# Kernel optimization log

Measured on AMD Instinct MI355X. Metric: run time of the kernel, lower is better.

The kernel has to match this reference:

```python
import jax, jax.numpy as jnp
import numpy as np

B, S, D, H, E, K = 4, 1024, 1024, 4096, 8, 2

def setup_inputs() -> dict:
    key = jax.random.key(0)
    ks = jax.random.split(key, 6)
    sd = 1.0 / np.sqrt(D)
    sh = 1.0 / np.sqrt(H)
    return {
        "x": jax.random.normal(ks[0], (B, S, D), jnp.float32),
        "Wg": jax.random.normal(ks[1], (D, E), jnp.float32) * sd,
        "bg": jnp.zeros((E,), jnp.float32),
        "W1": jax.random.normal(ks[2], (E, D, H), jnp.float32) * sd,
        "b1": jnp.zeros((E, H), jnp.float32),
        "Wa": jax.random.normal(ks[3], (E, D, H), jnp.float32) * sd,
        "ba": jnp.zeros((E, H), jnp.float32),
        "W2": jax.random.normal(ks[4], (E, H, D), jnp.float32) * sh,
        "b2": jnp.zeros((E, D), jnp.float32),
        "kv_cache": 0,
    }

def reference(x, Wg, bg, W1, b1, Wa, ba, W2, b2, kv_cache):
    # gate: softmax over experts, top-k, renormalize
    gate = jax.nn.softmax(x @ Wg + bg, axis=-1)            # [B,S,E]
    w, idx = jax.lax.top_k(gate, K)                        # [B,S,K]
    w = w / jnp.sum(w, axis=-1, keepdims=True)
    # dense all-expert FF with SwiGLU: fc2( silu(fc_a(x)) * fc1(x) )
    a = jnp.einsum('bsd,edh->bseh', x, Wa) + ba            # [B,S,E,H]
    g = a * jax.nn.sigmoid(a)
    u = jnp.einsum('bsd,edh->bseh', x, W1) + b1
    y = jnp.einsum('bseh,ehd->bsed', g * u, W2) + b2       # [B,S,E,D]
    # gather top-k experts per token and combine
    sel = jnp.take_along_axis(y, idx[..., None], axis=2)   # [B,S,K,D]
    out = jnp.sum(sel * w[..., None], axis=-2)             # [B,S,D]
    return out
```

## Files before the change

### kernel.cpp

```cpp
#include <hip/hip_runtime.h>
#include <hip/hip_bf16.h>
#include <math.h>

#define TOKENS 4096
#define DD 1024
#define HH 4096
#define NE 8
#define PAIRS 8192
#define ROWCAP 8448
#define TILE_CAP 40
#define G1_NT 16
#define G2_NT 32

typedef __bf16 bf16x8 __attribute__((ext_vector_type(8)));
typedef float f32x4 __attribute__((ext_vector_type(4)));

__device__ __forceinline__ unsigned short f2bf(float f) {
  union { float f; unsigned int u; } c; c.f = f;
  unsigned int x = c.u;
  return (unsigned short)((x + 0x7fffu + ((x >> 16) & 1u)) >> 16);
}

__device__ __forceinline__ void lds16(void* l, const void* g) {
  __builtin_amdgcn_global_load_lds((const __attribute__((address_space(1))) void*)g,
                                   (__attribute__((address_space(3))) void*)l, 16, 0, 0);
}

__global__ void init_kernel(int* counts) {
  if (threadIdx.x < NE) counts[threadIdx.x] = 0;
}

__global__ __launch_bounds__(256) void transpose_kernel(const float* __restrict__ in,
                                                        unsigned short* __restrict__ out,
                                                        int R, int C) {
  int ntr = R >> 6, ntc = C >> 6;
  int per_e = ntr * ntc;
  int b = blockIdx.x;
  int e = b / per_e;
  int rem = b - e * per_e;
  int tr = rem / ntc, tc = rem - (rem / ntc) * ntc;
  const float* ie = in + (size_t)e * R * C;
  unsigned short* oe = out + (size_t)e * R * C;

  __shared__ float t[64][68];
  int tid = threadIdx.x;
  int lr = tid >> 2;
  int c4 = (tid & 3) << 4;
  const float* src = ie + (size_t)(tr * 64 + lr) * C + tc * 64 + c4;
  float4 v0 = *(const float4*)(src);
  float4 v1 = *(const float4*)(src + 4);
  float4 v2 = *(const float4*)(src + 8);
  float4 v3 = *(const float4*)(src + 12);
  *(float4*)&t[lr][c4] = v0;
  *(float4*)&t[lr][c4 + 4] = v1;
  *(float4*)&t[lr][c4 + 8] = v2;
  *(float4*)&t[lr][c4 + 12] = v3;
  __syncthreads();

  int oc = tid >> 2;
  int r0 = (tid & 3) << 4;
  unsigned int pk[8];
#pragma unroll
  for (int i = 0; i < 8; i++) {
    unsigned int lo = f2bf(t[r0 + 2 * i][oc]);
    unsigned int hi = f2bf(t[r0 + 2 * i + 1][oc]);
    pk[i] = lo | (hi << 16);
  }
  unsigned short* dst = oe + (size_t)(tc * 64 + oc) * R + tr * 64 + r0;
  *(uint4*)(dst) = make_uint4(pk[0], pk[1], pk[2], pk[3]);
  *(uint4*)(dst + 8) = make_uint4(pk[4], pk[5], pk[6], pk[7]);
}

__global__ __launch_bounds__(256) void gate_kernel(const float* __restrict__ x,
    const float* __restrict__ Wg, const float* __restrict__ bg,
    int* __restrict__ counts, int* __restrict__ tok_e, int* __restrict__ tok_slot,
    float* __restrict__ tok_w) {
  int t = blockIdx.x, tid = threadIdx.x;
  const float* xr = x + (size_t)t * DD;
  float p[8] = {0, 0, 0, 0, 0, 0, 0, 0};
  for (int d = tid; d < DD; d += 256) {
    float xv = xr[d];
    const float4* wrow = (const float4*)(Wg + (size_t)d * NE);
    float4 w0 = wrow[0], w1 = wrow[1];
    p[0] += xv * w0.x; p[1] += xv * w0.y; p[2] += xv * w0.z; p[3] += xv * w0.w;
    p[4] += xv * w1.x; p[5] += xv * w1.y; p[6] += xv * w1.z; p[7] += xv * w1.w;
  }
#pragma unroll
  for (int e = 0; e < 8; e++) {
    p[e] += __shfl_down(p[e], 32);
    p[e] += __shfl_down(p[e], 16);
    p[e] += __shfl_down(p[e], 8);
    p[e] += __shfl_down(p[e], 4);
    p[e] += __shfl_down(p[e], 2);
    p[e] += __shfl_down(p[e], 1);
  }
  __shared__ float red[4][8];
  if ((tid & 63) == 0) {
#pragma unroll
    for (int e = 0; e < 8; e++) red[tid >> 6][e] = p[e];
  }
  __syncthreads();
  if (tid == 0) {
    float l[8];
#pragma unroll
    for (int e = 0; e < 8; e++) l[e] = red[0][e] + red[1][e] + red[2][e] + red[3][e] + bg[e];
    int e0 = 0; float l0 = l[0];
    for (int e = 1; e < 8; e++) if (l[e] > l0) { e0 = e; l0 = l[e]; }
    int e1 = -1; float l1 = -3.4e38f;
    for (int e = 0; e < 8; e++) if (e != e0 && l[e] > l1) { e1 = e; l1 = l[e]; }
    float w0 = 1.f / (1.f + __expf(l1 - l0));
    float w1 = 1.f - w0;
    int s0 = atomicAdd(&counts[e0], 1);
    int s1 = atomicAdd(&counts[e1], 1);
    tok_e[2 * t] = e0;     tok_slot[2 * t] = s0;     tok_w[2 * t] = w0;
    tok_e[2 * t + 1] = e1; tok_slot[2 * t + 1] = s1; tok_w[2 * t + 1] = w1;
  }
}

__global__ void scan_kernel(const int* __restrict__ counts, int* __restrict__ offsets,
                            int* __restrict__ tm_e, int* __restrict__ tm_row0,
                            int* __restrict__ tm_nrow, int* __restrict__ ntp) {
  if (threadIdx.x != 0 || blockIdx.x != 0) return;
  int c[NE];
#pragma unroll
  for (int e = 0; e < NE; e++) c[e] = counts[e];
  int off = 0, nt = 0;
  for (int e = 0; e < NE; e++) {
    offsets[e] = off;
    for (int r = 0; r < c[e]; r += 256) {
      tm_e[nt] = e;
      tm_row0[nt] = off + r;
      tm_nrow[nt] = (c[e] - r < 256) ? (c[e] - r) : 256;
      nt++;
    }
    off += c[e];
  }
  *ntp = nt;
}

__global__ __launch_bounds__(64) void gather_kernel(const float* __restrict__ x,
    const int* __restrict__ tok_e, const int* __restrict__ tok_slot,
    const float* __restrict__ tok_w, const int* __restrict__ offsets,
    unsigned short* __restrict__ Xe, int* __restrict__ pair_row, float* __restrict__ rw) {
  int pp = blockIdx.x, tid = threadIdx.x;
  int e = tok_e[pp];
  int row = offsets[e] + tok_slot[pp];
  int t = pp >> 1;
  const float* src = x + (size_t)t * DD + tid * 16;
  float4 v0 = *(const float4*)(src);
  float4 v1 = *(const float4*)(src + 4);
  float4 v2 = *(const float4*)(src + 8);
  float4 v3 = *(const float4*)(src + 12);
  unsigned int pk[8];
  pk[0] = f2bf(v0.x) | ((unsigned int)f2bf(v0.y) << 16);
  pk[1] = f2bf(v0.z) | ((unsigned int)f2bf(v0.w) << 16);
  pk[2] = f2bf(v1.x) | ((unsigned int)f2bf(v1.y) << 16);
  pk[3] = f2bf(v1.z) | ((unsigned int)f2bf(v1.w) << 16);
  pk[4] = f2bf(v2.x) | ((unsigned int)f2bf(v2.y) << 16);
  pk[5] = f2bf(v2.z) | ((unsigned int)f2bf(v2.w) << 16);
  pk[6] = f2bf(v3.x) | ((unsigned int)f2bf(v3.y) << 16);
  pk[7] = f2bf(v3.z) | ((unsigned int)f2bf(v3.w) << 16);
  unsigned short* dst = Xe + (size_t)row * DD + tid * 16;
  *(uint4*)(dst) = make_uint4(pk[0], pk[1], pk[2], pk[3]);
  *(uint4*)(dst + 8) = make_uint4(pk[4], pk[5], pk[6], pk[7]);
  if (tid == 0) { pair_row[pp] = row; rw[row] = tok_w[pp]; }
}

__global__ __launch_bounds__(512, 2) void gemm1_kernel(
    const unsigned short* __restrict__ Xe,
    const unsigned short* __restrict__ WaT,
    const unsigned short* __restrict__ W1T,
    const float* __restrict__ ba, const float* __restrict__ b1,
    unsigned short* __restrict__ h,
    const int* __restrict__ tm_e, const int* __restrict__ tm_row0,
    const int* __restrict__ tm_nrow, const int* __restrict__ ntp) {
  __shared__ unsigned short sm[8][8192];

  int work = blockIdx.x;
  int tile = work >> 5;
  if (tile >= *ntp) return;
  int n0 = (work & 31) << 7;
  int e = tm_e[tile], row0 = tm_row0[tile], nrow = tm_nrow[tile];

  int tid = threadIdx.x;
  int lane = tid & 63, wid = tid >> 6;
  int wm = wid >> 2, wn = wid & 3;
  int fr = lane & 15, kc = lane >> 4;

  const unsigned short* gA  = Xe + (size_t)row0 * DD;
  const unsigned short* gA1 = gA + (size_t)128 * DD;
  const unsigned short* gBa = WaT + ((size_t)e << 22) + (size_t)n0 * DD;
  const unsigned short* gBu = W1T + ((size_t)e << 22) + (size_t)n0 * DD;

  int srow = tid >> 3;
  int sx0 = (((tid & 7) ^ (srow & 7)) << 3);

  auto stg = [&](int tt, int slot, const unsigned short* gsrc) {
    int c = tt < G1_NT ? tt : G1_NT - 1;
    unsigned short* L = &sm[((tt & 1) << 2) | slot][0];
    const unsigned short* s = gsrc + (size_t)srow * DD + (c << 6) + sx0;
    lds16(L + (size_t)tid * 8, s);
    lds16(L + (size_t)(tid + 512) * 8, s + (size_t)64 * DD);
  };
  auto fragp = [&](int buf, int slot, int r, int ks) {
    return (const bf16x8*)(&sm[(buf << 2) | slot][0] + r * 64 +
                           ((((ks << 2) | kc) ^ (r & 7)) << 3));
  };

  f32x4 accA[8][2], accU[8][2];
  f32x4 z = {0.f, 0.f, 0.f, 0.f};
#pragma unroll
  for (int m = 0; m < 8; m++)
#pragma unroll
    for (int n = 0; n < 2; n++) { accA[m][n] = z; accU[m][n] = z; }

  stg(0, 2, gBa); stg(0, 3, gBu); stg(0, 0, gA); stg(0, 1, gA1);
  stg(1, 2, gBa); stg(1, 3, gBu); stg(1, 0, gA);
  asm volatile("s_waitcnt vmcnt(6)\ns_barrier" ::: "memory");

  for (int T = 0; T < G1_NT; ++T) {
    int buf = T & 1;
    bf16x8 a[4][2], bA[2][2], bU[2][2];
#pragma unroll
    for (int m = 0; m < 4; m++)
#pragma unroll
      for (int ks = 0; ks < 2; ks++) {
        int R = wm * 128 + m * 16 + fr;
        a[m][ks] = *fragp(buf, R >> 7, R & 127, ks);
      }
#pragma unroll
    for (int n = 0; n < 2; n++)
#pragma unroll
      for (int ks = 0; ks < 2; ks++)
        bA[n][ks] = *fragp(buf, 2, wn * 32 + n * 16 + fr, ks);
    stg(T + 1, 1, gA1);
    __builtin_amdgcn_s_setprio(1);
#pragma unroll
    for (int m = 0; m < 4; m++)
#pragma unroll
      for (int n = 0; n < 2; n++)
#pragma unroll
        for (int ks = 0; ks < 2; ks++)
          accA[m][n] = __builtin_amdgcn_mfma_f32_16x16x32_bf16(a[m][ks], bA[n][ks], accA[m][n], 0, 0, 0);
    __builtin_amdgcn_s_setprio(0);
    asm volatile("s_waitcnt lgkmcnt(0)\ns_barrier" ::: "memory");
#pragma unroll
    for (int n = 0; n < 2; n++)
#pragma unroll
      for (int ks = 0; ks < 2; ks++)
        bU[n][ks] = *fragp(buf, 3, wn * 32 + n * 16 + fr, ks);
    stg(T + 2, 2, gBa);
    __builtin_amdgcn_s_setprio(1);
#pragma unroll
    for (int m = 0; m < 4; m++)
#pragma unroll
      for (int n = 0; n < 2; n++)
#pragma unroll
        for (int ks = 0; ks < 2; ks++)
          accU[m][n] = __builtin_amdgcn_mfma_f32_16x16x32_bf16(a[m][ks], bU[n][ks], accU[m][n], 0, 0, 0);
    __builtin_amdgcn_s_setprio(0);
    asm volatile("s_waitcnt lgkmcnt(0)\ns_barrier" ::: "memory");
#pragma unroll
    for (int m = 0; m < 4; m++)
#pragma unroll
      for (int ks = 0; ks < 2; ks++) {
        int R = wm * 128 + 64 + m * 16 + fr;
        a[m][ks] = *fragp(buf, R >> 7, R & 127, ks);
      }
    stg(T + 2, 3, gBu);
    __builtin_amdgcn_s_setprio(1);
#pragma unroll
    for (int m = 0; m < 4; m++)
#pragma unroll
      for (int n = 0; n < 2; n++)
#pragma unroll
        for (int ks = 0; ks < 2; ks++)
          accA[4 + m][n] = __builtin_amdgcn_mfma_f32_16x16x32_bf16(a[m][ks], bA[n][ks], accA[4 + m][n], 0, 0, 0);
    __builtin_amdgcn_s_setprio(0);
    asm volatile("s_waitcnt lgkmcnt(0)\ns_barrier" ::: "memory");
    stg(T + 2, 0, gA);
    __builtin_amdgcn_s_setprio(1);
#pragma unroll
    for (int m = 0; m < 4; m++)
#pragma unroll
      for (int n = 0; n < 2; n++)
#pragma unroll
        for (int ks = 0; ks < 2; ks++)
          accU[4 + m][n] = __builtin_amdgcn_mfma_f32_16x16x32_bf16(a[m][ks], bU[n][ks], accU[4 + m][n], 0, 0, 0);
    __builtin_amdgcn_s_setprio(0);
    asm volatile("s_waitcnt vmcnt(6)\ns_barrier" ::: "memory");
  }

  int lr4 = kc * 4;
#pragma unroll
  for (int n = 0; n < 2; n++) {
    int col = n0 + wn * 32 + n * 16 + fr;
    float bav = ba[e * HH + col];
    float buv = b1[e * HH + col];
#pragma unroll
    for (int m = 0; m < 8; m++) {
#pragma unroll
      for (int j = 0; j < 4; j++) {
        int r = wm * 128 + m * 16 + lr4 + j;
        if (r < nrow) {
          float av = accA[m][n][j] + bav;
          float uv = accU[m][n][j] + buv;
          float s = __builtin_amdgcn_rcpf(1.f + __expf(-av));
          h[(size_t)(row0 + r) * HH + col] = f2bf(av * s * uv);
        }
      }
    }
  }
}

__global__ __launch_bounds__(512, 2) void gemm2_kernel(
    const unsigned short* __restrict__ hb,
    const unsigned short* __restrict__ W2T,
    const float* __restrict__ b2, const float* __restrict__ rw,
    float* __restrict__ contribA, float* __restrict__ contribB,
    const int* __restrict__ tm_e, const int* __restrict__ tm_row0,
    const int* __restrict__ tm_nrow, const int* __restrict__ ntp) {
  __shared__ unsigned short sm[9][8192];

  int work = blockIdx.x;
  int tile = work >> 4;
  if (tile >= *ntp) return;
  int rem = work & 15;
  int n0 = (rem >> 1) << 7;
  int kh = rem & 1;
  int e = tm_e[tile], row0 = tm_row0[tile], nrow = tm_nrow[tile];

  int tid = threadIdx.x;
  int lane = tid & 63, wid = tid >> 6;
  int wm = wid >> 2, wn = wid & 3;
  int fr = lane & 15, kc = lane >> 4;

  const unsigned short* gA = hb + (size_t)row0 * HH + kh * 2048;
  const unsigned short* gB = W2T + ((size_t)e << 22) + (size_t)n0 * HH + kh * 2048;

  int srow = tid >> 3;
  int sx0 = (((tid & 7) ^ (srow & 7)) << 3);

  auto stgA = [&](int tt) {
    int c = tt < G2_NT ? tt : G2_NT - 1;
    int sl = (tt % 3) << 1;
    const unsigned short* s = gA + (size_t)srow * HH + (c << 6) + sx0;
    lds16(&sm[sl][0] + (size_t)tid * 8, s);
    lds16(&sm[sl][0] + (size_t)(tid + 512) * 8, s + (size_t)64 * HH);
    lds16(&sm[sl + 1][0] + (size_t)tid * 8, s + (size_t)128 * HH);
    lds16(&sm[sl + 1][0] + (size_t)(tid + 512) * 8, s + (size_t)192 * HH);
  };
  auto stgB = [&](int tt) {
    int c = tt < G2_NT ? tt : G2_NT - 1;
    unsigned short* L = &sm[6 + tt % 3][0];
    const unsigned short* s = gB + (size_t)srow * HH + (c << 6) + sx0;
    lds16(L + (size_t)tid * 8, s);
    lds16(L + (size_t)(tid + 512) * 8, s + (size_t)64 * HH);
  };
  auto fragp = [&](int slot, int r, int ks) {
    return (const bf16x8*)(&sm[slot][0] + r * 64 + ((((ks << 2) | kc) ^ (r & 7)) << 3));
  };

  f32x4 acc[8][2];
  f32x4 z = {0.f, 0.f, 0.f, 0.f};
#pragma unroll
  for (int m = 0; m < 8; m++)
#pragma unroll
    for (int n = 0; n < 2; n++) acc[m][n] = z;

  stgB(0); stgA(0); stgB(1); stgA(1); stgB(2);
  asm volatile("s_waitcnt vmcnt(6)\ns_barrier" ::: "memory");

  for (int T = 0; T < G2_NT; ++T) {
    int slA = (T % 3) << 1;
    int slB = 6 + T % 3;
    bf16x8 a[4][2], b[2][2];
#pragma unroll
    for (int m = 0; m < 4; m++)
#pragma unroll
      for (int ks = 0; ks < 2; ks++) {
        int R = wm * 128 + m * 16 + fr;
        a[m][ks] = *fragp(slA + (R >> 7), R & 127, ks);
      }
#pragma unroll
    for (int n = 0; n < 2; n++)
#pragma unroll
      for (int ks = 0; ks < 2; ks++)
        b[n][ks] = *fragp(slB, wn * 32 + n * 16 + fr, ks);
    stgA(T + 2);
    __builtin_amdgcn_s_setprio(1);
#pragma unroll
    for (int m = 0; m < 4; m++)
#pragma unroll
      for (int n = 0; n < 2; n++)
#pragma unroll
        for (int ks = 0; ks < 2; ks++)
          acc[m][n] = __builtin_amdgcn_mfma_f32_16x16x32_bf16(a[m][ks], b[n][ks], acc[m][n], 0, 0, 0);
    __builtin_amdgcn_s_setprio(0);
    asm volatile("s_waitcnt lgkmcnt(0)\ns_barrier" ::: "memory");
#pragma unroll
    for (int m = 0; m < 4; m++)
#pragma unroll
      for (int ks = 0; ks < 2; ks++) {
        int R = wm * 128 + 64 + m * 16 + fr;
        a[m][ks] = *fragp(slA + (R >> 7), R & 127, ks);
      }
    stgB(T + 3);
    __builtin_amdgcn_s_setprio(1);
#pragma unroll
    for (int m = 0; m < 4; m++)
#pragma unroll
      for (int n = 0; n < 2; n++)
#pragma unroll
        for (int ks = 0; ks < 2; ks++)
          acc[4 + m][n] = __builtin_amdgcn_mfma_f32_16x16x32_bf16(a[m][ks], b[n][ks], acc[4 + m][n], 0, 0, 0);
    __builtin_amdgcn_s_setprio(0);
    asm volatile("s_waitcnt vmcnt(6) lgkmcnt(0)\ns_barrier" ::: "memory");
  }

  float b2v[2];
#pragma unroll
  for (int n = 0; n < 2; n++)
    b2v[n] = (kh == 0) ? b2[e * DD + n0 + wn * 32 + n * 16 + fr] : 0.f;
  float* cbuf = kh ? contribB : contribA;
  int lr4 = kc * 4;
#pragma unroll
  for (int m = 0; m < 8; m++) {
#pragma unroll
    for (int j = 0; j < 4; j++) {
      int r = wm * 128 + m * 16 + lr4 + j;
      if (r < nrow) {
        float wv = rw[row0 + r];
        float* dst = cbuf + (size_t)(row0 + r) * DD + n0 + wn * 32 + fr;
        dst[0]  = wv * (acc[m][0][j] + b2v[0]);
        dst[16] = wv * (acc[m][1][j] + b2v[1]);
      }
    }
  }
}

__global__ __launch_bounds__(256) void combine_kernel(const float* __restrict__ cA,
    const float* __restrict__ cB, const int* __restrict__ pair_row,
    float* __restrict__ out) {
  int t = blockIdx.x, tid = threadIdx.x;
  int r0 = pair_row[2 * t], r1 = pair_row[2 * t + 1];
  const float4* a0 = (const float4*)(cA + (size_t)r0 * DD);
  const float4* b0 = (const float4*)(cB + (size_t)r0 * DD);
  const float4* a1 = (const float4*)(cA + (size_t)r1 * DD);
  const float4* b1 = (const float4*)(cB + (size_t)r1 * DD);
  float4* o = (float4*)(out + (size_t)t * DD);
  float4 x0 = a0[tid], y0 = b0[tid], x1 = a1[tid], y1 = b1[tid];
  o[tid] = make_float4((x0.x + y0.x) + (x1.x + y1.x),
                       (x0.y + y0.y) + (x1.y + y1.y),
                       (x0.z + y0.z) + (x1.z + y1.z),
                       (x0.w + y0.w) + (x1.w + y1.w));
}

extern "C" void kernel_launch(void* const* d_in, const int* in_sizes, int n_in,
                              void* d_out, int out_size, void* d_ws, size_t ws_size,
                              hipStream_t stream) {
  const float* x  = (const float*)d_in[0];
  const float* Wg = (const float*)d_in[1];
  const float* bg = (const float*)d_in[2];
  const float* W1 = (const float*)d_in[3];
  const float* b1 = (const float*)d_in[4];
  const float* Wa = (const float*)d_in[5];
  const float* ba = (const float*)d_in[6];
  const float* W2 = (const float*)d_in[7];
  const float* b2 = (const float*)d_in[8];
  float* out = (float*)d_out;
  (void)in_sizes; (void)n_in; (void)out_size; (void)ws_size;

  char* p = (char*)d_ws;
  auto take = [&](size_t bytes) { char* r = p; p += (bytes + 255) & ~(size_t)255; return r; };
  unsigned short* WaT = (unsigned short*)take((size_t)NE * HH * DD * 2);
  unsigned short* W1T = (unsigned short*)take((size_t)NE * HH * DD * 2);
  unsigned short* W2T = (unsigned short*)take((size_t)NE * DD * HH * 2);
  unsigned short* Xe  = (unsigned short*)take((size_t)ROWCAP * DD * 2);
  unsigned short* hb  = (unsigned short*)take((size_t)ROWCAP * HH * 2);
  float* contribA     = (float*)take((size_t)ROWCAP * DD * 4);
  int* counts   = (int*)take(64);
  int* offsets  = (int*)take(64);
  int* tok_e    = (int*)take(PAIRS * 4);
  int* tok_slot = (int*)take(PAIRS * 4);
  float* tok_w  = (float*)take(PAIRS * 4);
  int* pair_row = (int*)take(PAIRS * 4);
  float* rw     = (float*)take(ROWCAP * 4);
  int* tm_e     = (int*)take(TILE_CAP * 4);
  int* tm_row0  = (int*)take(TILE_CAP * 4);
  int* tm_nrow  = (int*)take(TILE_CAP * 4);
  int* ntp      = (int*)take(64);
  float* contribB = (float*)WaT;

  init_kernel<<<1, 64, 0, stream>>>(counts);
  transpose_kernel<<<NE * 16 * 64, 256, 0, stream>>>(Wa, WaT, DD, HH);
  transpose_kernel<<<NE * 16 * 64, 256, 0, stream>>>(W1, W1T, DD, HH);
  transpose_kernel<<<NE * 64 * 16, 256, 0, stream>>>(W2, W2T, HH, DD);
  gate_kernel<<<TOKENS, 256, 0, stream>>>(x, Wg, bg, counts, tok_e, tok_slot, tok_w);
  scan_kernel<<<1, 64, 0, stream>>>(counts, offsets, tm_e, tm_row0, tm_nrow, ntp);
  gather_kernel<<<PAIRS, 64, 0, stream>>>(x, tok_e, tok_slot, tok_w, offsets, Xe, pair_row, rw);
  gemm1_kernel<<<TILE_CAP * 32, 512, 0, stream>>>(Xe, WaT, W1T, ba, b1, hb, tm_e, tm_row0, tm_nrow, ntp);
  gemm2_kernel<<<TILE_CAP * 16, 512, 0, stream>>>(hb, W2T, b2, rw, contribA, contribB, tm_e, tm_row0, tm_nrow, ntp);
  combine_kernel<<<TOKENS, 256, 0, stream>>>(contribA, contribB, pair_row, out);
}
```

Before: 533.4 us.

## Retile gemm2 to 128x256 tiles and restructure barrier/MFMA scheduling in both GEMMs

gemm2 now uses its own 128-row expert tile map and 128x256 output tiles (wider N, fewer rows), with separate double-buffered A and triple-buffered B LDS stages. Both GEMMs move the barrier before the MFMA bursts, wait on LDS reads just before compute, add sched_barrier fences, and reorder MFMA loops with ks outermost. The goal is to cut padding waste on partially filled 256-row expert tiles in gemm2, improve operand reuse, and let memory and compute overlap better. In exchange there are more barriers per iteration and a different LDS footprint, which may change occupancy.

Result: slower. 587.2 us (+10.1%).

```diff
diff --git a/kernel.cpp b/kernel.cpp
--- a/kernel.cpp
+++ b/kernel.cpp
@@ -8,7 +8,8 @@
 #define NE 8
 #define PAIRS 8192
 #define ROWCAP 8448
-#define TILE_CAP 40
+#define T1CAP 40
+#define T2CAP 72
 #define G1_NT 16
 #define G2_NT 32
 
@@ -118,24 +119,31 @@
 }
 
 __global__ void scan_kernel(const int* __restrict__ counts, int* __restrict__ offsets,
-                            int* __restrict__ tm_e, int* __restrict__ tm_row0,
-                            int* __restrict__ tm_nrow, int* __restrict__ ntp) {
+                            int* __restrict__ tm1_e, int* __restrict__ tm1_row0,
+                            int* __restrict__ tm1_nrow, int* __restrict__ ntp1,
+                            int* __restrict__ tm2_e, int* __restrict__ tm2_row0,
+                            int* __restrict__ tm2_nrow, int* __restrict__ ntp2) {
   if (threadIdx.x != 0 || blockIdx.x != 0) return;
   int c[NE];
 #pragma unroll
   for (int e = 0; e < NE; e++) c[e] = counts[e];
-  int off = 0, nt = 0;
+  int off = 0, n1 = 0, n2 = 0;
   for (int e = 0; e < NE; e++) {
     offsets[e] = off;
     for (int r = 0; r < c[e]; r += 256) {
-      tm_e[nt] = e;
-      tm_row0[nt] = off + r;
-      tm_nrow[nt] = (c[e] - r < 256) ? (c[e] - r) : 256;
-      nt++;
+      tm1_e[n1] = e; tm1_row0[n1] = off + r;
+      tm1_nrow[n1] = (c[e] - r < 256) ? (c[e] - r) : 256;
+      n1++;
+    }
+    for (int r = 0; r < c[e]; r += 128) {
+      tm2_e[n2] = e; tm2_row0[n2] = off + r;
+      tm2_nrow[n2] = (c[e] - r < 128) ? (c[e] - r) : 128;
+      n2++;
     }
     off += c[e];
   }
-  *ntp = nt;
+  *ntp1 = n1;
+  *ntp2 = n2;
 }
 
 __global__ __launch_bounds__(64) void gather_kernel(const float* __restrict__ x,
@@ -216,7 +224,8 @@
 
   stg(0, 2, gBa); stg(0, 3, gBu); stg(0, 0, gA); stg(0, 1, gA1);
   stg(1, 2, gBa); stg(1, 3, gBu); stg(1, 0, gA);
-  asm volatile("s_waitcnt vmcnt(6)\ns_barrier" ::: "memory");
+  asm volatile("s_waitcnt vmcnt(6)" ::: "memory");
+  __builtin_amdgcn_s_barrier();
 
   for (int T = 0; T < G1_NT; ++T) {
     int buf = T & 1;
@@ -234,32 +243,38 @@
       for (int ks = 0; ks < 2; ks++)
         bA[n][ks] = *fragp(buf, 2, wn * 32 + n * 16 + fr, ks);
     stg(T + 1, 1, gA1);
+    __builtin_amdgcn_s_barrier();
+    asm volatile("s_waitcnt lgkmcnt(0)" ::: "memory");
+    __builtin_amdgcn_sched_barrier(0);
     __builtin_amdgcn_s_setprio(1);
 #pragma unroll
-    for (int m = 0; m < 4; m++)
-#pragma unroll
-      for (int n = 0; n < 2; n++)
-#pragma unroll
-        for (int ks = 0; ks < 2; ks++)
+    for (int ks = 0; ks < 2; ks++)
+#pragma unroll
+      for (int m = 0; m < 4; m++)
+#pragma unroll
+        for (int n = 0; n < 2; n++)
           accA[m][n] = __builtin_amdgcn_mfma_f32_16x16x32_bf16(a[m][ks], bA[n][ks], accA[m][n], 0, 0, 0);
     __builtin_amdgcn_s_setprio(0);
-    asm volatile("s_waitcnt lgkmcnt(0)\ns_barrier" ::: "memory");
+    __builtin_amdgcn_s_barrier();
 #pragma unroll
     for (int n = 0; n < 2; n++)
 #pragma unroll
       for (int ks = 0; ks < 2; ks++)
         bU[n][ks] = *fragp(buf, 3, wn * 32 + n * 16 + fr, ks);
     stg(T + 2, 2, gBa);
+    __builtin_amdgcn_s_barrier();
+    asm volatile("s_waitcnt lgkmcnt(0)" ::: "memory");
+    __builtin_amdgcn_sched_barrier(0);
     __builtin_amdgcn_s_setprio(1);
 #pragma unroll
-    for (int m = 0; m < 4; m++)
-#pragma unroll
-      for (int n = 0; n < 2; n++)
-#pragma unroll
-        for (int ks = 0; ks < 2; ks++)
+    for (int ks = 0; ks < 2; ks++)
+#pragma unroll
+      for (int m = 0; m < 4; m++)
+#pragma unroll
+        for (int n = 0; n < 2; n++)
           accU[m][n] = __builtin_amdgcn_mfma_f32_16x16x32_bf16(a[m][ks], bU[n][ks], accU[m][n], 0, 0, 0);
     __builtin_amdgcn_s_setprio(0);
-    asm volatile("s_waitcnt lgkmcnt(0)\ns_barrier" ::: "memory");
+    __builtin_amdgcn_s_barrier();
 #pragma unroll
     for (int m = 0; m < 4; m++)
 #pragma unroll
@@ -268,27 +283,33 @@
         a[m][ks] = *fragp(buf, R >> 7, R & 127, ks);
       }
     stg(T + 2, 3, gBu);
+    __builtin_amdgcn_s_barrier();
+    asm volatile("s_waitcnt lgkmcnt(0)" ::: "memory");
+    __builtin_amdgcn_sched_barrier(0);
     __builtin_amdgcn_s_setprio(1);
 #pragma unroll
-    for (int m = 0; m < 4; m++)
-#pragma unroll
-      for (int n = 0; n < 2; n++)
-#pragma unroll
-        for (int ks = 0; ks < 2; ks++)
+    for (int ks = 0; ks < 2; ks++)
+#pragma unroll
+      for (int m = 0; m < 4; m++)
+#pragma unroll
+        for (int n = 0; n < 2; n++)
           accA[4 + m][n] = __builtin_amdgcn_mfma_f32_16x16x32_bf16(a[m][ks], bA[n][ks], accA[4 + m][n], 0, 0, 0);
     __builtin_amdgcn_s_setprio(0);
-    asm volatile("s_waitcnt lgkmcnt(0)\ns_barrier" ::: "memory");
+    __builtin_amdgcn_s_barrier();
     stg(T + 2, 0, gA);
+    __builtin_amdgcn_s_barrier();
+    __builtin_amdgcn_sched_barrier(0);
     __builtin_amdgcn_s_setprio(1);
 #pragma unroll
-    for (int m = 0; m < 4; m++)
-#pragma unroll
-      for (int n = 0; n < 2; n++)
-#pragma unroll
-        for (int ks = 0; ks < 2; ks++)
+    for (int ks = 0; ks < 2; ks++)
+#pragma unroll
+      for (int m = 0; m < 4; m++)
+#pragma unroll
+        for (int n = 0; n < 2; n++)
           accU[4 + m][n] = __builtin_amdgcn_mfma_f32_16x16x32_bf16(a[m][ks], bU[n][ks], accU[4 + m][n], 0, 0, 0);
     __builtin_amdgcn_s_setprio(0);
-    asm volatile("s_waitcnt vmcnt(6)\ns_barrier" ::: "memory");
+    asm volatile("s_waitcnt vmcnt(6)" ::: "memory");
+    __builtin_amdgcn_s_barrier();
   }
 
   int lr4 = kc * 4;
@@ -320,13 +341,14 @@
     float* __restrict__ contribA, float* __restrict__ contribB,
     const int* __restrict__ tm_e, const int* __restrict__ tm_row0,
     const int* __restrict__ tm_nrow, const int* __restrict__ ntp) {
-  __shared__ unsigned short sm[9][8192];
+  __shared__ unsigned short smA[2][8192];
+  __shared__ unsigned short smB[3][16384];
 
   int work = blockIdx.x;
-  int tile = work >> 4;
+  int tile = work >> 3;
   if (tile >= *ntp) return;
-  int rem = work & 15;
-  int n0 = (rem >> 1) << 7;
+  int rem = work & 7;
+  int n0 = (rem >> 1) << 8;
   int kh = rem & 1;
   int e = tm_e[tile], row0 = tm_row0[tile], nrow = tm_nrow[tile];
 
@@ -343,97 +365,104 @@
 
   auto stgA = [&](int tt) {
     int c = tt < G2_NT ? tt : G2_NT - 1;
-    int sl = (tt % 3) << 1;
+    unsigned short* L = &smA[tt & 1][0];
     const unsigned short* s = gA + (size_t)srow * HH + (c << 6) + sx0;
-    lds16(&sm[sl][0] + (size_t)tid * 8, s);
-    lds16(&sm[sl][0] + (size_t)(tid + 512) * 8, s + (size_t)64 * HH);
-    lds16(&sm[sl + 1][0] + (size_t)tid * 8, s + (size_t)128 * HH);
-    lds16(&sm[sl + 1][0] + (size_t)(tid + 512) * 8, s + (size_t)192 * HH);
+    lds16(L + (size_t)tid * 8, s);
+    lds16(L + (size_t)(tid + 512) * 8, s + (size_t)64 * HH);
   };
   auto stgB = [&](int tt) {
     int c = tt < G2_NT ? tt : G2_NT - 1;
-    unsigned short* L = &sm[6 + tt % 3][0];
+    unsigned short* L = &smB[tt % 3][0];
     const unsigned short* s = gB + (size_t)srow * HH + (c << 6) + sx0;
     lds16(L + (size_t)tid * 8, s);
     lds16(L + (size_t)(tid + 512) * 8, s + (size_t)64 * HH);
+    lds16(L + (size_t)(tid + 1024) * 8, s + (size_t)128 * HH);
+    lds16(L + (size_t)(tid + 1536) * 8, s + (size_t)192 * HH);
   };
-  auto fragp = [&](int slot, int r, int ks) {
-    return (const bf16x8*)(&sm[slot][0] + r * 64 + ((((ks << 2) | kc) ^ (r & 7)) << 3));
+  auto fragA = [&](int par, int r, int ks) {
+    return (const bf16x8*)(&smA[par][0] + r * 64 + ((((ks << 2) | kc) ^ (r & 7)) << 3));
   };
-
-  f32x4 acc[8][2];
+  auto fragB = [&](int slot, int r, int ks) {
+    return (const bf16x8*)(&smB[slot][0] + r * 64 + ((((ks << 2) | kc) ^ (r & 7)) << 3));
+  };
+
+  f32x4 acc[4][4];
   f32x4 z = {0.f, 0.f, 0.f, 0.f};
 #pragma unroll
-  for (int m = 0; m < 8; m++)
-#pragma unroll
-    for (int n = 0; n < 2; n++) acc[m][n] = z;
-
-  stgB(0); stgA(0); stgB(1); stgA(1); stgB(2);
-  asm volatile("s_waitcnt vmcnt(6)\ns_barrier" ::: "memory");
+  for (int m = 0; m < 4; m++)
+#pragma unroll
+    for (int n = 0; n < 4; n++) acc[m][n] = z;
+
+  stgB(0); stgA(0); stgB(1); stgA(1);
+  asm volatile("s_waitcnt vmcnt(6)" ::: "memory");
+  __builtin_amdgcn_s_barrier();
 
   for (int T = 0; T < G2_NT; ++T) {
-    int slA = (T % 3) << 1;
-    int slB = 6 + T % 3;
-    bf16x8 a[4][2], b[2][2];
+    int par = T & 1, slB = T % 3;
+    bf16x8 a[4][2], b[4][2];
 #pragma unroll
     for (int m = 0; m < 4; m++)
 #pragma unroll
-      for (int ks = 0; ks < 2; ks++) {
-        int R = wm * 128 + m * 16 + fr;
-        a[m][ks] = *fragp(slA + (R >> 7), R & 127, ks);
-      }
+      for (int ks = 0; ks < 2; ks++)
+        a[m][ks] = *fragA(par, wm * 64 + m * 16 + fr, ks);
 #pragma unroll
     for (int n = 0; n < 2; n++)
 #pragma unroll
       for (int ks = 0; ks < 2; ks++)
-        b[n][ks] = *fragp(slB, wn * 32 + n * 16 + fr, ks);
-    stgA(T + 2);
+        b[n][ks] = *fragB(slB, wn * 64 + n * 16 + fr, ks);
+    stgB(T + 2);
+    __builtin_amdgcn_s_barrier();
+    asm volatile("s_waitcnt lgkmcnt(0)" ::: "memory");
+    __builtin_amdgcn_sched_barrier(0);
     __builtin_amdgcn_s_setprio(1);
 #pragma unroll
-    for (int m = 0; m < 4; m++)
-#pragma unroll
-      for (int n = 0; n < 2; n++)
-#pragma unroll
-        for (int ks = 0; ks < 2; ks++)
+    for (int ks = 0; ks < 2; ks++)
+#pragma unroll
+      for (int m = 0; m < 4; m++)
+#pragma unroll
+        for (int n = 0; n < 2; n++)
           acc[m][n] = __builtin_amdgcn_mfma_f32_16x16x32_bf16(a[m][ks], b[n][ks], acc[m][n], 0, 0, 0);
     __builtin_amdgcn_s_setprio(0);
-    asm volatile("s_waitcnt lgkmcnt(0)\ns_barrier" ::: "memory");
-#pragma unroll
-    for (int m = 0; m < 4; m++)
-#pragma unroll
-      for (int ks = 0; ks < 2; ks++) {
-        int R = wm * 128 + 64 + m * 16 + fr;
-        a[m][ks] = *fragp(slA + (R >> 7), R & 127, ks);
-      }
-    stgB(T + 3);
+    __builtin_amdgcn_s_barrier();
+#pragma unroll
+    for (int n = 2; n < 4; n++)
+#pragma unroll
+      for (int ks = 0; ks < 2; ks++)
+        b[n][ks] = *fragB(slB, wn * 64 + n * 16 + fr, ks);
+    stgA(T + 2);
+    __builtin_amdgcn_s_barrier();
+    asm volatile("s_waitcnt lgkmcnt(0)" ::: "memory");
+    __builtin_amdgcn_sched_barrier(0);
     __builtin_amdgcn_s_setprio(1);
 #pragma unroll
-    for (int m = 0; m < 4; m++)
-#pragma unroll
-      for (int n = 0; n < 2; n++)
-#pragma unroll
-        for (int ks = 0; ks < 2; ks++)
-          acc[4 + m][n] = __builtin_amdgcn_mfma_f32_16x16x32_bf16(a[m][ks], b[n][ks], acc[4 + m][n], 0, 0, 0);
+    for (int ks = 0; ks < 2; ks++)
+#pragma unroll
+      for (int m = 0; m < 4; m++)
+#pragma unroll
+        for (int n = 2; n < 4; n++)
+          acc[m][n] = __builtin_amdgcn_mfma_f32_16x16x32_bf16(a[m][ks], b[n][ks], acc[m][n], 0, 0, 0);
     __builtin_amdgcn_s_setprio(0);
-    asm volatile("s_waitcnt vmcnt(6) lgkmcnt(0)\ns_barrier" ::: "memory");
-  }
-
-  float b2v[2];
-#pragma unroll
-  for (int n = 0; n < 2; n++)
-    b2v[n] = (kh == 0) ? b2[e * DD + n0 + wn * 32 + n * 16 + fr] : 0.f;
+    asm volatile("s_waitcnt vmcnt(6)" ::: "memory");
+    __builtin_amdgcn_s_barrier();
+  }
+
+  float b2v[4];
+#pragma unroll
+  for (int n = 0; n < 4; n++)
+    b2v[n] = (kh == 0) ? b2[e * DD + n0 + wn * 64 + n * 16 + fr] : 0.f;
   float* cbuf = kh ? contribB : contribA;
   int lr4 = kc * 4;
 #pragma unroll
-  for (int m = 0; m < 8; m++) {
+  for (int m = 0; m < 4; m++) {
 #pragma unroll
     for (int j = 0; j < 4; j++) {
-      int r = wm * 128 + m * 16 + lr4 + j;
+      int r = wm * 64 + m * 16 + lr4 + j;
       if (r < nrow) {
         float wv = rw[row0 + r];
-        float* dst = cbuf + (size_t)(row0 + r) * DD + n0 + wn * 32 + fr;
-        dst[0]  = wv * (acc[m][0][j] + b2v[0]);
-        dst[16] = wv * (acc[m][1][j] + b2v[1]);
+        float* dst = cbuf + (size_t)(row0 + r) * DD + n0 + wn * 64 + fr;
+#pragma unroll
+        for (int n = 0; n < 4; n++)
+          dst[n * 16] = wv * (acc[m][n][j] + b2v[n]);
       }
     }
   }
@@ -486,10 +515,14 @@
   float* tok_w  = (float*)take(PAIRS * 4);
   int* pair_row = (int*)take(PAIRS * 4);
   float* rw     = (float*)take(ROWCAP * 4);
-  int* tm_e     = (int*)take(TILE_CAP * 4);
-  int* tm_row0  = (int*)take(TILE_CAP * 4);
-  int* tm_nrow  = (int*)take(TILE_CAP * 4);
-  int* ntp      = (int*)take(64);
+  int* tm1_e    = (int*)take(T1CAP * 4);
+  int* tm1_row0 = (int*)take(T1CAP * 4);
+  int* tm1_nrow = (int*)take(T1CAP * 4);
+  int* ntp1     = (int*)take(64);
+  int* tm2_e    = (int*)take(T2CAP * 4);
+  int* tm2_row0 = (int*)take(T2CAP * 4);
+  int* tm2_nrow = (int*)take(T2CAP * 4);
+  int* ntp2     = (int*)take(64);
   float* contribB = (float*)WaT;
 
   init_kernel<<<1, 64, 0, stream>>>(counts);
@@ -497,9 +530,10 @@
   transpose_kernel<<<NE * 16 * 64, 256, 0, stream>>>(W1, W1T, DD, HH);
   transpose_kernel<<<NE * 64 * 16, 256, 0, stream>>>(W2, W2T, HH, DD);
   gate_kernel<<<TOKENS, 256, 0, stream>>>(x, Wg, bg, counts, tok_e, tok_slot, tok_w);
-  scan_kernel<<<1, 64, 0, stream>>>(counts, offsets, tm_e, tm_row0, tm_nrow, ntp);
+  scan_kernel<<<1, 64, 0, stream>>>(counts, offsets, tm1_e, tm1_row0, tm1_nrow, ntp1,
+                                    tm2_e, tm2_row0, tm2_nrow, ntp2);
   gather_kernel<<<PAIRS, 64, 0, stream>>>(x, tok_e, tok_slot, tok_w, offsets, Xe, pair_row, rw);
-  gemm1_kernel<<<TILE_CAP * 32, 512, 0, stream>>>(Xe, WaT, W1T, ba, b1, hb, tm_e, tm_row0, tm_nrow, ntp);
-  gemm2_kernel<<<TILE_CAP * 16, 512, 0, stream>>>(hb, W2T, b2, rw, contribA, contribB, tm_e, tm_row0, tm_nrow, ntp);
+  gemm1_kernel<<<T1CAP * 32, 512, 0, stream>>>(Xe, WaT, W1T, ba, b1, hb, tm1_e, tm1_row0, tm1_nrow, ntp1);
+  gemm2_kernel<<<T2CAP * 8, 512, 0, stream>>>(hb, W2T, b2, rw, contribA, contribB, tm2_e, tm2_row0, tm2_nrow, ntp2);
   combine_kernel<<<TOKENS, 256, 0, stream>>>(contribA, contribB, pair_row, out);
 }
```
